# Kernel tuning notes

Measured on AMD Instinct MI355X. Metric: run time of the kernel, lower is better.

The kernel has to match this reference:

```python
import jax, jax.numpy as jnp
import numpy as np
import math

HIDDEN = 1024
N_HEADS = 16
N_KV = 4
HEAD_DIM = HIDDEN // N_HEADS  # 64
B, S = 2, 2048
THETA = 100000.0


def _freqs_cos_sin(dim, end, theta):
    # yarn params: original_max_position_embeddings=2048 >= end, so no ramp scaling,
    # attention_factor=1.0 -> plain RoPE frequencies.
    inv = 1.0 / theta ** (np.arange(0, dim, 2)[: dim // 2] / dim)
    t = np.arange(end)
    f = np.outer(t, inv).astype(np.float32)  # (end, dim/2)
    cos = np.concatenate([np.cos(f), np.cos(f)], axis=-1)  # (end, dim)
    sin = np.concatenate([np.sin(f), np.sin(f)], axis=-1)
    return jnp.asarray(cos), jnp.asarray(sin)


def _rotate(x):
    # stack([-x[...,1::2], x[...,::2]], -1).reshape_as(x)
    return jnp.stack([-x[..., 1::2], x[..., ::2]], axis=-1).reshape(x.shape)


def setup_inputs() -> dict:
    key = jax.random.key(0)
    ks = jax.random.split(key, 9)
    s = 0.02
    return {
        "hidden_states": jax.random.normal(ks[0], (B, S, HIDDEN), jnp.float32),
        "attention_mask": jnp.ones((B, S), jnp.int32),
        "Wq": jax.random.normal(ks[1], (HIDDEN, HIDDEN), jnp.float32) * s,
        "bq": jnp.zeros((HIDDEN,), jnp.float32),
        "Wk": jax.random.normal(ks[2], (HIDDEN, N_KV * HEAD_DIM), jnp.float32) * s,
        "bk": jnp.zeros((N_KV * HEAD_DIM,), jnp.float32),
        "Wv": jax.random.normal(ks[3], (HIDDEN, N_KV * HEAD_DIM), jnp.float32) * s,
        "bv": jnp.zeros((N_KV * HEAD_DIM,), jnp.float32),
        "Wo": jax.random.normal(ks[4], (HIDDEN, HIDDEN), jnp.float32) * s,
        "bo": jnp.zeros((HIDDEN,), jnp.float32),
    }


def reference(hidden_states, attention_mask, Wq, bq, Wk, bk, Wv, bv, Wo, bo):
    b, s, _ = hidden_states.shape
    q = (hidden_states @ Wq + bq).reshape(b, s, N_HEADS, HEAD_DIM)
    k = (hidden_states @ Wk + bk).reshape(b, s, N_KV, HEAD_DIM)
    v = (hidden_states @ Wv + bv).reshape(b, s, N_KV, HEAD_DIM)

    cos, sin = _freqs_cos_sin(HEAD_DIM, s, THETA)
    cos = cos[:, None, :]  # (s,1,d) broadcasts over (b,s,h,d)
    sin = sin[:, None, :]
    q = q * cos + _rotate(q) * sin
    k = k * cos + _rotate(k) * sin

    # GQA: repeat_interleave kv heads -> jnp.repeat along head axis
    rep = N_HEADS // N_KV
    k = jnp.repeat(k, rep, axis=2)
    v = jnp.repeat(v, rep, axis=2)

    scores = jnp.einsum("bqhd,bkhd->bhqk", q, k) / math.sqrt(HEAD_DIM)
    neg = jnp.finfo(scores.dtype).min
    causal = jnp.triu(jnp.ones((s, s), bool), k=1)  # (q,kv)
    bias = jnp.where(causal, neg, 0.0).astype(scores.dtype)[None, None]
    key_mask = attention_mask.astype(bool)[:, None, None, :]  # (b,1,1,kv)
    bias = jnp.where(key_mask, bias, neg)
    probs = jax.nn.softmax(scores + bias, axis=-1)
    attn = jnp.einsum("bhqk,bkhd->bqhd", probs, v).reshape(b, s, HIDDEN)
    return attn @ Wo + bo
```

## Files before the change

kernel.cpp:

```cpp
#include <hip/hip_runtime.h>
#include <cstddef>
#include <cstdint>

#define B_   2
#define S_   2048
#define HID  1024
#define NH_  16
#define NKV_ 4
#define DH_  64
#define ROWS (B_ * S_)
#define NQKV 1536
#define QSCALE 0.18033688011112042f

typedef __bf16 bf16_t;
typedef _Float16 f16_t;
typedef bf16_t bf16x8 __attribute__((ext_vector_type(8)));
typedef bf16_t bf16x4 __attribute__((ext_vector_type(4)));
typedef f16_t  f16x8  __attribute__((ext_vector_type(8)));
typedef f16_t  f16x4  __attribute__((ext_vector_type(4)));
typedef float  f32x4  __attribute__((ext_vector_type(4)));

typedef __attribute__((address_space(1))) const uint32_t gu32_t;
typedef __attribute__((address_space(3))) uint32_t lu32_t;

__device__ __forceinline__ void gl_lds16(const void* g, void* l) {
  __builtin_amdgcn_global_load_lds((gu32_t*)g, (lu32_t*)l, 16, 0, 0);
}

__global__ void prep_all(const float* __restrict__ hs,
                         const float* __restrict__ Wq, const float* __restrict__ Wk,
                         const float* __restrict__ Wv, const float* __restrict__ Wo,
                         const float* __restrict__ bq, const float* __restrict__ bk,
                         const float* __restrict__ bv,
                         bf16_t* __restrict__ hsb,
                         bf16_t* __restrict__ Wt, bf16_t* __restrict__ Wot,
                         float* __restrict__ ball, float2* __restrict__ lut)
{
  const int bid = blockIdx.x;
  if (bid < 2048) {
    const int i = (bid * 256 + threadIdx.x) * 8;
    float4 a = *(const float4*)(hs + i);
    float4 b = *(const float4*)(hs + i + 4);
    bf16x8 o;
    o[0]=(bf16_t)a.x; o[1]=(bf16_t)a.y; o[2]=(bf16_t)a.z; o[3]=(bf16_t)a.w;
    o[4]=(bf16_t)b.x; o[5]=(bf16_t)b.y; o[6]=(bf16_t)b.z; o[7]=(bf16_t)b.w;
    *(bf16x8*)(hsb + i) = o;
    return;
  }
  if (bid >= 4614) {
    const int idx = (bid - 4614) * 256 + threadIdx.x;
    const int s = idx >> 5, j = idx & 31;
    const float L = 0.51905126482615037f;
    const float ang = (float)s * exp2f(-L * (float)j);
    lut[idx] = make_float2(cosf(ang), sinf(ang));
    return;
  }
  if (bid >= 4608) {
    int i = (bid - 4608) * 256 + threadIdx.x;
    if (i < NQKV) ball[i] = (i < 1024) ? bq[i] : ((i < 1280) ? bk[i-1024] : bv[i-1280]);
    return;
  }
  const int wb = bid - 2048;
  const float* src; bf16_t* dst; int N, n0, k0;
  if (wb < 1024)      { src = Wq; dst = Wt;            N = 1024; int t = wb;      n0=(t&31)*32; k0=(t>>5)*32; }
  else if (wb < 1280) { src = Wk; dst = Wt + 1024*HID; N = 256;  int t = wb-1024; n0=(t&7)*32;  k0=(t>>3)*32; }
  else if (wb < 1536) { src = Wv; dst = Wt + 1280*HID; N = 256;  int t = wb-1280; n0=(t&7)*32;  k0=(t>>3)*32; }
  else                { src = Wo; dst = Wot;           N = 1024; int t = wb-1536; n0=(t&31)*32; k0=(t>>5)*32; }
  __shared__ bf16_t T[32][33];
  const int tx = threadIdx.x & 31, ty = threadIdx.x >> 5;
#pragma unroll
  for (int i = 0; i < 4; ++i)
    T[ty + i*8][tx] = (bf16_t)src[(size_t)(k0 + ty + i*8) * N + n0 + tx];
  __syncthreads();
#pragma unroll
  for (int i = 0; i < 4; ++i)
    dst[(size_t)(n0 + ty + i*8) * HID + k0 + tx] = T[tx][ty + i*8];
}

__global__ __launch_bounds__(256, 3) void gemm64_b16o(
    const bf16_t* __restrict__ A, const bf16_t* __restrict__ Bt,
    const float* __restrict__ bias, bf16_t* __restrict__ C, int N)
{
  __shared__ bf16_t As[128 * 64];
  __shared__ bf16_t Bs[64 * 64];
  const int tid  = threadIdx.x;
  const int w    = tid >> 6;
  const int lane = tid & 63;
  const int m    = lane & 15;
  const int quad = lane >> 4;
  const int wm   = w >> 1, wn = w & 1;
  const size_t bm = (size_t)blockIdx.y * 128;
  const size_t bn = (size_t)blockIdx.x * 64;

  const int srow = w * 8 + (lane >> 3);
  const int scol = (lane & 7) * 8;
  const bf16_t* Ag = A  + (bm + srow) * HID + scol;
  const bf16_t* Bg = Bt + (bn + srow) * HID + scol;

  f32x4 acc[4][2];
#pragma unroll
  for (int i = 0; i < 4; ++i)
#pragma unroll
    for (int j = 0; j < 2; ++j) acc[i][j] = (f32x4){0.f, 0.f, 0.f, 0.f};

  for (int k0 = 0; k0 < HID; k0 += 64) {
    __syncthreads();
#pragma unroll
    for (int i = 0; i < 4; ++i)
      gl_lds16(Ag + (size_t)(i * 32) * HID + k0, &As[(w * 8 + i * 32) * 64]);
#pragma unroll
    for (int i = 0; i < 2; ++i)
      gl_lds16(Bg + (size_t)(i * 32) * HID + k0, &Bs[(w * 8 + i * 32) * 64]);
    __syncthreads();
#pragma unroll
    for (int ks = 0; ks < 2; ++ks) {
      bf16x8 af[4], bfr[2];
#pragma unroll
      for (int mt = 0; mt < 4; ++mt)
        af[mt] = *(const bf16x8*)&As[(wm * 64 + mt * 16 + m) * 64 + ks * 32 + quad * 8];
#pragma unroll
      for (int nt = 0; nt < 2; ++nt)
        bfr[nt] = *(const bf16x8*)&Bs[(wn * 32 + nt * 16 + m) * 64 + ks * 32 + quad * 8];
#pragma unroll
      for (int mt = 0; mt < 4; ++mt)
#pragma unroll
        for (int nt = 0; nt < 2; ++nt)
          acc[mt][nt] = __builtin_amdgcn_mfma_f32_16x16x32_bf16(bfr[nt], af[mt], acc[mt][nt], 0, 0, 0);
    }
  }
#pragma unroll
  for (int mt = 0; mt < 4; ++mt) {
    const size_t row = bm + wm * 64 + mt * 16 + m;
#pragma unroll
    for (int nt = 0; nt < 2; ++nt) {
      const size_t col = bn + wn * 32 + nt * 16 + quad * 4;
      float4 bb = *(const float4*)&bias[col];
      bf16x4 o;
      o[0] = (bf16_t)(acc[mt][nt][0] + bb.x);
      o[1] = (bf16_t)(acc[mt][nt][1] + bb.y);
      o[2] = (bf16_t)(acc[mt][nt][2] + bb.z);
      o[3] = (bf16_t)(acc[mt][nt][3] + bb.w);
      *(bf16x4*)&C[row * N + col] = o;
    }
  }
}

__global__ __launch_bounds__(256, 3) void gemm64_f32o(
    const bf16_t* __restrict__ A, const bf16_t* __restrict__ Bt,
    const float* __restrict__ bias, float* __restrict__ C, int N)
{
  __shared__ bf16_t As[128 * 64];
  __shared__ bf16_t Bs[64 * 64];
  const int tid  = threadIdx.x;
  const int w    = tid >> 6;
  const int lane = tid & 63;
  const int m    = lane & 15;
  const int quad = lane >> 4;
  const int wm   = w >> 1, wn = w & 1;
  const size_t bm = (size_t)blockIdx.y * 128;
  const size_t bn = (size_t)blockIdx.x * 64;

  const int srow = w * 8 + (lane >> 3);
  const int scol = (lane & 7) * 8;
  const bf16_t* Ag = A  + (bm + srow) * HID + scol;
  const bf16_t* Bg = Bt + (bn + srow) * HID + scol;

  f32x4 acc[4][2];
#pragma unroll
  for (int i = 0; i < 4; ++i)
#pragma unroll
    for (int j = 0; j < 2; ++j) acc[i][j] = (f32x4){0.f, 0.f, 0.f, 0.f};

  for (int k0 = 0; k0 < HID; k0 += 64) {
    __syncthreads();
#pragma unroll
    for (int i = 0; i < 4; ++i)
      gl_lds16(Ag + (size_t)(i * 32) * HID + k0, &As[(w * 8 + i * 32) * 64]);
#pragma unroll
    for (int i = 0; i < 2; ++i)
      gl_lds16(Bg + (size_t)(i * 32) * HID + k0, &Bs[(w * 8 + i * 32) * 64]);
    __syncthreads();
#pragma unroll
    for (int ks = 0; ks < 2; ++ks) {
      bf16x8 af[4], bfr[2];
#pragma unroll
      for (int mt = 0; mt < 4; ++mt)
        af[mt] = *(const bf16x8*)&As[(wm * 64 + mt * 16 + m) * 64 + ks * 32 + quad * 8];
#pragma unroll
      for (int nt = 0; nt < 2; ++nt)
        bfr[nt] = *(const bf16x8*)&Bs[(wn * 32 + nt * 16 + m) * 64 + ks * 32 + quad * 8];
#pragma unroll
      for (int mt = 0; mt < 4; ++mt)
#pragma unroll
        for (int nt = 0; nt < 2; ++nt)
          acc[mt][nt] = __builtin_amdgcn_mfma_f32_16x16x32_bf16(bfr[nt], af[mt], acc[mt][nt], 0, 0, 0);
    }
  }
#pragma unroll
  for (int mt = 0; mt < 4; ++mt) {
    const size_t row = bm + wm * 64 + mt * 16 + m;
#pragma unroll
    for (int nt = 0; nt < 2; ++nt) {
      const size_t col = bn + wn * 32 + nt * 16 + quad * 4;
      float4 bb = *(const float4*)&bias[col];
      float4 o;
      o.x = acc[mt][nt][0] + bb.x; o.y = acc[mt][nt][1] + bb.y;
      o.z = acc[mt][nt][2] + bb.z; o.w = acc[mt][nt][3] + bb.w;
      *(float4*)&C[row * N + col] = o;
    }
  }
}

__global__ void prep_kv(const bf16_t* __restrict__ QKVb, const float2* __restrict__ lut,
                        bf16_t* __restrict__ Kimg, f16_t* __restrict__ Vimg)
{
  __shared__ bf16_t Lk[64][72];
  __shared__ bf16_t Lv[64][72];
  const int bid = blockIdx.x, t = threadIdx.x;
  const int kt = bid & 31, kvh = (bid >> 5) & 3, b = bid >> 7;
  const size_t img = ((size_t)(b * NKV_ + kvh) * 32 + kt) * 4096;

  {
    const int r0 = t >> 3, c8 = (t & 7) * 8;
#pragma unroll
    for (int i = 0; i < 2; ++i) {
      const int r = r0 + i * 32;
      const bf16_t* src = QKVb + (size_t)(b * S_ + kt * 64 + r) * NQKV + 1024 + kvh * DH_ + c8;
      *(bf16x8*)&Lk[r][c8] = *(const bf16x8*)src;
      *(bf16x8*)&Lv[r][c8] = *(const bf16x8*)(src + 256);
    }
  }
  __syncthreads();
  {
    const int key = t & 63, cg = t >> 6;
    const int srow = kt * 64 + key;
    bf16x8 a = *(const bf16x8*)&Lk[key][cg * 16];
    bf16x8 c = *(const bf16x8*)&Lk[key][cg * 16 + 8];
    const float2* lp = lut + srow * 32 + ((cg & 1) * 16);
    float v[16];
#pragma unroll
    for (int i = 0; i < 8; ++i) { v[i] = (float)a[i]; v[i + 8] = (float)c[i]; }
    bf16x8 o0, o1;
#pragma unroll
    for (int j = 0; j < 8; ++j) {
      const float2 ce = lp[2 * j], co = lp[2 * j + 1];
      const float y0 = v[2*j] * ce.x - v[2*j+1] * ce.y;
      const float y1 = v[2*j+1] * co.x + v[2*j] * co.y;
      if (j < 4) { o0[2*j] = (bf16_t)y0; o0[2*j+1] = (bf16_t)y1; }
      else       { o1[2*(j-4)] = (bf16_t)y0; o1[2*(j-4)+1] = (bf16_t)y1; }
    }
    const int s0 = (2 * cg) ^ (key & 7);
    *(bf16x8*)&Kimg[img + key * 64 + s0 * 8]       = o0;
    *(bf16x8*)&Kimg[img + key * 64 + (s0 ^ 1) * 8] = o1;
  }
  {
    const int d = t & 63, cg = t >> 6;
#pragma unroll
    for (int g4 = 0; g4 < 4; ++g4) {
      const int g = cg * 4 + g4;
      f16x4 o;
#pragma unroll
      for (int j = 0; j < 4; ++j)
        o[j] = (f16_t)(float)Lv[g * 4 + j][d];
      const int slot = g ^ (d & 15);
      *(f16x4*)&Vimg[img + d * 64 + slot * 4] = o;
    }
  }
}

__global__ __launch_bounds__(64) void attn_v5(
    const bf16_t* __restrict__ QKVb, const float2* __restrict__ lut,
    const bf16_t* __restrict__ Kt2, const f16_t* __restrict__ Vt2,
    const int* __restrict__ amask, bf16_t* __restrict__ Ab)
{
  __shared__ __align__(16) bf16_t Ks[64 * 64];
  __shared__ __align__(16) f16_t  Vs[64 * 64];

  const int lane = threadIdx.x;
  const int m    = lane & 15;
  const int quad = lane >> 4;
  const int h    = blockIdx.y;
  const int b    = blockIdx.z;
  const int kvh  = h >> 2;
  const int qt   = 63 - blockIdx.x;
  const int q0w  = qt * 32;
  const int nkt  = ((q0w + 31) >> 6) + 1;

  bf16x8 aq[2][2];
#pragma unroll
  for (int mt = 0; mt < 2; ++mt) {
    const int spos = q0w + mt * 16 + m;
    const bf16_t* qsrc = QKVb + (size_t)(b * S_ + spos) * NQKV + h * DH_;
    float2 l8[8];
#pragma unroll
    for (int j = 0; j < 8; ++j) l8[j] = lut[spos * 32 + quad * 8 + j];
#pragma unroll
    for (int kc = 0; kc < 2; ++kc) {
      bf16x8 x = *(const bf16x8*)(qsrc + kc * 32 + quad * 8);
      bf16x8 y;
#pragma unroll
      for (int i = 0; i < 4; ++i) {
        const float x0 = (float)x[2*i], x1 = (float)x[2*i+1];
        y[2*i]   = (bf16_t)((x0 * l8[2*i].x   - x1 * l8[2*i].y)   * QSCALE);
        y[2*i+1] = (bf16_t)((x1 * l8[2*i+1].x + x0 * l8[2*i+1].y) * QSCALE);
      }
      aq[mt][kc] = y;
    }
  }

  f32x4 oacc[2][4];
#pragma unroll
  for (int mt = 0; mt < 2; ++mt)
#pragma unroll
    for (int d = 0; d < 4; ++d) oacc[mt][d] = (f32x4){0.f,0.f,0.f,0.f};
  float lpart[2] = {0.f, 0.f};

  const size_t imgbase = ((size_t)(b * NKV_ + kvh) * 32) * 4096;
  const bf16_t* Kg = Kt2 + imgbase;
  const f16_t*  Vg = Vt2 + imgbase;
  const int x0s = quad ^ (m & 7);
  const int x1s = (4 + quad) ^ (m & 7);
  const int* amp = amask + b * S_;

  for (int kt = 0; kt < nkt; ++kt) {
    const int kbase = kt * 64;
#pragma unroll
    for (int i = 0; i < 8; ++i)
      gl_lds16(Kg + (size_t)kt * 4096 + i * 512 + lane * 8, &Ks[i * 512]);
#pragma unroll
    for (int i = 0; i < 8; ++i)
      gl_lds16(Vg + (size_t)kt * 4096 + i * 512 + lane * 8, &Vs[i * 512]);

    const uint64_t mb = __ballot(amp[kbase + lane] != 0);
    __builtin_amdgcn_s_waitcnt(0x0F70);

    f32x4 sc[2][4];
#pragma unroll
    for (int mt = 0; mt < 2; ++mt)
#pragma unroll
      for (int cb = 0; cb < 4; ++cb) sc[mt][cb] = (f32x4){0.f,0.f,0.f,0.f};
#pragma unroll
    for (int cb = 0; cb < 4; ++cb) {
      const bf16x8 bk0 = *(const bf16x8*)&Ks[(cb*16 + m) * 64 + x0s * 8];
      const bf16x8 bk1 = *(const bf16x8*)&Ks[(cb*16 + m) * 64 + x1s * 8];
#pragma unroll
      for (int mt = 0; mt < 2; ++mt) {
        sc[mt][cb] = __builtin_amdgcn_mfma_f32_16x16x32_bf16(bk0, aq[mt][0], sc[mt][cb], 0, 0, 0);
        sc[mt][cb] = __builtin_amdgcn_mfma_f32_16x16x32_bf16(bk1, aq[mt][1], sc[mt][cb], 0, 0, 0);
      }
    }

    f16x4 bp[2][4];
#pragma unroll
    for (int mt = 0; mt < 2; ++mt) {
      const bool needm = (kbase + 63 > q0w + mt*16) || (mb != ~0ull);
      if (needm) {
        const int qv = q0w + mt*16 + m;
#pragma unroll
        for (int cb = 0; cb < 4; ++cb)
#pragma unroll
          for (int r = 0; r < 4; ++r) {
            const int idx = cb*16 + quad*4 + r;
            const bool ok = (kbase + idx <= qv) && ((mb >> idx) & 1);
            sc[mt][cb][r] = ok ? sc[mt][cb][r] : -1e38f;
          }
      }
      float sum = 0.f;
#pragma unroll
      for (int cb = 0; cb < 4; ++cb) {
        f16x4 pp;
#pragma unroll
        for (int r = 0; r < 4; ++r) {
          const float p = exp2f(sc[mt][cb][r]);
          sum += p;
          pp[r] = (f16_t)p;
        }
        bp[mt][cb] = pp;
      }
      lpart[mt] += sum;
    }

#pragma unroll
    for (int cb = 0; cb < 4; ++cb) {
      f16x4 av[4];
#pragma unroll
      for (int dblk = 0; dblk < 4; ++dblk) {
        const int slot = (cb * 4 + quad) ^ m;
        av[dblk] = *(const f16x4*)&Vs[(dblk*16 + m) * 64 + slot * 4];
      }
#pragma unroll
      for (int mt = 0; mt < 2; ++mt)
#pragma unroll
        for (int dblk = 0; dblk < 4; ++dblk)
          oacc[mt][dblk] = __builtin_amdgcn_mfma_f32_16x16x16f16(av[dblk], bp[mt][cb], oacc[mt][dblk], 0, 0, 0);
    }
  }

#pragma unroll
  for (int mt = 0; mt < 2; ++mt) {
    float l = lpart[mt];
    l += __shfl_xor(l, 16);
    l += __shfl_xor(l, 32);
    const float inv = 1.0f / l;
    const size_t row = (size_t)(b * S_ + q0w + mt*16 + m);
#pragma unroll
    for (int dblk = 0; dblk < 4; ++dblk) {
      bf16x4 o;
      o[0] = (bf16_t)(oacc[mt][dblk][0] * inv);
      o[1] = (bf16_t)(oacc[mt][dblk][1] * inv);
      o[2] = (bf16_t)(oacc[mt][dblk][2] * inv);
      o[3] = (bf16_t)(oacc[mt][dblk][3] * inv);
      *(bf16x4*)&Ab[row * HID + h * DH_ + dblk * 16 + quad * 4] = o;
    }
  }
}

extern "C" void kernel_launch(void* const* d_in, const int* in_sizes, int n_in,
                              void* d_out, int out_size, void* d_ws, size_t ws_size,
                              hipStream_t stream)
{
  const float* hs    = (const float*)d_in[0];
  const int*   amask = (const int*)  d_in[1];
  const float* Wq    = (const float*)d_in[2];
  const float* bq    = (const float*)d_in[3];
  const float* Wk    = (const float*)d_in[4];
  const float* bk    = (const float*)d_in[5];
  const float* Wv    = (const float*)d_in[6];
  const float* bv    = (const float*)d_in[7];
  const float* Wo    = (const float*)d_in[8];
  const float* bo    = (const float*)d_in[9];
  float* out = (float*)d_out;

  bf16_t* QKVb = (bf16_t*)d_ws;
  bf16_t* hsb  = QKVb + (size_t)ROWS * NQKV;
  bf16_t* Wt   = hsb + (size_t)ROWS * HID;
  bf16_t* Wot  = Wt + (size_t)NQKV * HID;
  float*  ball = (float*)(Wot + (size_t)HID * HID);
  bf16_t* Kimg = (bf16_t*)(ball + NQKV);
  f16_t*  Vimg = (f16_t*)(Kimg + (size_t)B_*NKV_*32*4096);
  float2* lut  = (float2*)(Vimg + (size_t)B_*NKV_*32*4096);
  bf16_t* Ab   = hsb;

  prep_all<<<4870, 256, 0, stream>>>(hs, Wq, Wk, Wv, Wo, bq, bk, bv,
                                     hsb, Wt, Wot, ball, lut);

  gemm64_b16o<<<dim3(NQKV/64, ROWS/128), 256, 0, stream>>>(hsb, Wt, ball, QKVb, NQKV);

  prep_kv<<<256, 256, 0, stream>>>(QKVb, lut, Kimg, Vimg);

  attn_v5<<<dim3(64, NH_, B_), 64, 0, stream>>>(QKVb, lut, Kimg, Vimg, amask, Ab);

  gemm64_f32o<<<dim3(HID/64, ROWS/128), 256, 0, stream>>>(Ab, Wot, bo, out, HID);
}
```

Before: 212.7 us.

## Load K/V MFMA fragments directly into registers with double-buffered prefetch

The attention kernel no longer stages K/V tiles through LDS. Each lane now loads its MFMA fragments straight from global memory into registers, using two register buffers so the next tile's loads overlap the current tile's compute. prep_kv rewrites the K and V images into a fragment-friendly unswizzled layout so each lane's reads are contiguous, and it reads K directly from global memory instead of through shared memory. This removes the LDS round trip and waitcnt stalls, at the cost of more VGPRs for two fragment sets, which could lower occupancy.

```diff
diff --git a/kernel.cpp b/kernel.cpp
--- a/kernel.cpp
+++ b/kernel.cpp
@@ -214,7 +214,6 @@
 __global__ void prep_kv(const bf16_t* __restrict__ QKVb, const float2* __restrict__ lut,
                         bf16_t* __restrict__ Kimg, f16_t* __restrict__ Vimg)
 {
-  __shared__ bf16_t Lk[64][72];
   __shared__ bf16_t Lv[64][72];
   const int bid = blockIdx.x, t = threadIdx.x;
   const int kt = bid & 31, kvh = (bid >> 5) & 3, b = bid >> 7;
@@ -225,17 +224,16 @@
 #pragma unroll
     for (int i = 0; i < 2; ++i) {
       const int r = r0 + i * 32;
-      const bf16_t* src = QKVb + (size_t)(b * S_ + kt * 64 + r) * NQKV + 1024 + kvh * DH_ + c8;
-      *(bf16x8*)&Lk[r][c8] = *(const bf16x8*)src;
-      *(bf16x8*)&Lv[r][c8] = *(const bf16x8*)(src + 256);
-    }
-  }
-  __syncthreads();
+      const bf16_t* src = QKVb + (size_t)(b * S_ + kt * 64 + r) * NQKV + 1280 + kvh * DH_ + c8;
+      *(bf16x8*)&Lv[r][c8] = *(const bf16x8*)src;
+    }
+  }
   {
     const int key = t & 63, cg = t >> 6;
     const int srow = kt * 64 + key;
-    bf16x8 a = *(const bf16x8*)&Lk[key][cg * 16];
-    bf16x8 c = *(const bf16x8*)&Lk[key][cg * 16 + 8];
+    const bf16_t* p = QKVb + (size_t)(b * S_ + srow) * NQKV + 1024 + kvh * DH_ + cg * 16;
+    bf16x8 a = *(const bf16x8*)p;
+    bf16x8 c = *(const bf16x8*)(p + 8);
     const float2* lp = lut + srow * 32 + ((cg & 1) * 16);
     float v[16];
 #pragma unroll
@@ -249,10 +247,10 @@
       if (j < 4) { o0[2*j] = (bf16_t)y0; o0[2*j+1] = (bf16_t)y1; }
       else       { o1[2*(j-4)] = (bf16_t)y0; o1[2*(j-4)+1] = (bf16_t)y1; }
     }
-    const int s0 = (2 * cg) ^ (key & 7);
-    *(bf16x8*)&Kimg[img + key * 64 + s0 * 8]       = o0;
-    *(bf16x8*)&Kimg[img + key * 64 + (s0 ^ 1) * 8] = o1;
-  }
+    *(bf16x8*)&Kimg[img + key * 64 + cg * 16]     = o0;
+    *(bf16x8*)&Kimg[img + key * 64 + cg * 16 + 8] = o1;
+  }
+  __syncthreads();
   {
     const int d = t & 63, cg = t >> 6;
 #pragma unroll
@@ -262,20 +260,97 @@
 #pragma unroll
       for (int j = 0; j < 4; ++j)
         o[j] = (f16_t)(float)Lv[g * 4 + j][d];
-      const int slot = g ^ (d & 15);
-      *(f16x4*)&Vimg[img + d * 64 + slot * 4] = o;
-    }
-  }
-}
-
-__global__ __launch_bounds__(64) void attn_v5(
+      *(f16x4*)&Vimg[img + (d * 4 + (g & 3)) * 16 + (g >> 2) * 4] = o;
+    }
+  }
+}
+
+struct KVFrag {
+  bf16x8 k[4][2];
+  f16x4  v[4][4];
+};
+
+__device__ __forceinline__ void load_frags(const bf16_t* __restrict__ Kg,
+                                           const f16_t* __restrict__ Vg,
+                                           int kt, int m, int quad, KVFrag& f)
+{
+  const bf16_t* kp = Kg + (size_t)kt * 4096 + m * 64 + quad * 8;
+#pragma unroll
+  for (int cb = 0; cb < 4; ++cb)
+#pragma unroll
+    for (int kc = 0; kc < 2; ++kc)
+      f.k[cb][kc] = *(const bf16x8*)(kp + cb * 1024 + kc * 32);
+  const f16_t* vp = Vg + (size_t)kt * 4096 + (m * 4 + quad) * 16;
+#pragma unroll
+  for (int dblk = 0; dblk < 4; ++dblk)
+#pragma unroll
+    for (int c2 = 0; c2 < 2; ++c2) {
+      f16x8 t = *(const f16x8*)(vp + dblk * 1024 + c2 * 8);
+      f.v[dblk][c2*2]   = __builtin_shufflevector(t, t, 0, 1, 2, 3);
+      f.v[dblk][c2*2+1] = __builtin_shufflevector(t, t, 4, 5, 6, 7);
+    }
+}
+
+__device__ __forceinline__ void tile_compute(const KVFrag& f, int mreg, int kbase,
+    int q0w, int m, int quad, const bf16x8 (&aq)[2][2],
+    f32x4 (&oacc)[2][4], float (&lpart)[2])
+{
+  const uint64_t mb = __ballot(mreg != 0);
+  f32x4 sc[2][4];
+#pragma unroll
+  for (int mt = 0; mt < 2; ++mt)
+#pragma unroll
+    for (int cb = 0; cb < 4; ++cb) sc[mt][cb] = (f32x4){0.f,0.f,0.f,0.f};
+#pragma unroll
+  for (int cb = 0; cb < 4; ++cb)
+#pragma unroll
+    for (int mt = 0; mt < 2; ++mt) {
+      sc[mt][cb] = __builtin_amdgcn_mfma_f32_16x16x32_bf16(f.k[cb][0], aq[mt][0], sc[mt][cb], 0, 0, 0);
+      sc[mt][cb] = __builtin_amdgcn_mfma_f32_16x16x32_bf16(f.k[cb][1], aq[mt][1], sc[mt][cb], 0, 0, 0);
+    }
+  f16x4 bp[2][4];
+#pragma unroll
+  for (int mt = 0; mt < 2; ++mt) {
+    const bool needm = (kbase + 63 > q0w + mt*16) || (mb != ~0ull);
+    if (needm) {
+      const int qv = q0w + mt*16 + m;
+#pragma unroll
+      for (int cb = 0; cb < 4; ++cb)
+#pragma unroll
+        for (int r = 0; r < 4; ++r) {
+          const int idx = cb*16 + quad*4 + r;
+          const bool ok = (kbase + idx <= qv) && ((mb >> idx) & 1);
+          sc[mt][cb][r] = ok ? sc[mt][cb][r] : -1e38f;
+        }
+    }
+    float sum = 0.f;
+#pragma unroll
+    for (int cb = 0; cb < 4; ++cb) {
+      f16x4 pp;
+#pragma unroll
+      for (int r = 0; r < 4; ++r) {
+        const float p = exp2f(sc[mt][cb][r]);
+        sum += p;
+        pp[r] = (f16_t)p;
+      }
+      bp[mt][cb] = pp;
+    }
+    lpart[mt] += sum;
+  }
+#pragma unroll
+  for (int cb = 0; cb < 4; ++cb)
+#pragma unroll
+    for (int mt = 0; mt < 2; ++mt)
+#pragma unroll
+      for (int dblk = 0; dblk < 4; ++dblk)
+        oacc[mt][dblk] = __builtin_amdgcn_mfma_f32_16x16x16f16(f.v[dblk][cb], bp[mt][cb], oacc[mt][dblk], 0, 0, 0);
+}
+
+__global__ __launch_bounds__(64) void attn_v7(
     const bf16_t* __restrict__ QKVb, const float2* __restrict__ lut,
     const bf16_t* __restrict__ Kt2, const f16_t* __restrict__ Vt2,
     const int* __restrict__ amask, bf16_t* __restrict__ Ab)
 {
-  __shared__ __align__(16) bf16_t Ks[64 * 64];
-  __shared__ __align__(16) f16_t  Vs[64 * 64];
-
   const int lane = threadIdx.x;
   const int m    = lane & 15;
   const int quad = lane >> 4;
@@ -318,82 +393,19 @@
   const size_t imgbase = ((size_t)(b * NKV_ + kvh) * 32) * 4096;
   const bf16_t* Kg = Kt2 + imgbase;
   const f16_t*  Vg = Vt2 + imgbase;
-  const int x0s = quad ^ (m & 7);
-  const int x1s = (4 + quad) ^ (m & 7);
   const int* amp = amask + b * S_;
 
-  for (int kt = 0; kt < nkt; ++kt) {
-    const int kbase = kt * 64;
-#pragma unroll
-    for (int i = 0; i < 8; ++i)
-      gl_lds16(Kg + (size_t)kt * 4096 + i * 512 + lane * 8, &Ks[i * 512]);
-#pragma unroll
-    for (int i = 0; i < 8; ++i)
-      gl_lds16(Vg + (size_t)kt * 4096 + i * 512 + lane * 8, &Vs[i * 512]);
-
-    const uint64_t mb = __ballot(amp[kbase + lane] != 0);
-    __builtin_amdgcn_s_waitcnt(0x0F70);
-
-    f32x4 sc[2][4];
-#pragma unroll
-    for (int mt = 0; mt < 2; ++mt)
-#pragma unroll
-      for (int cb = 0; cb < 4; ++cb) sc[mt][cb] = (f32x4){0.f,0.f,0.f,0.f};
-#pragma unroll
-    for (int cb = 0; cb < 4; ++cb) {
-      const bf16x8 bk0 = *(const bf16x8*)&Ks[(cb*16 + m) * 64 + x0s * 8];
-      const bf16x8 bk1 = *(const bf16x8*)&Ks[(cb*16 + m) * 64 + x1s * 8];
-#pragma unroll
-      for (int mt = 0; mt < 2; ++mt) {
-        sc[mt][cb] = __builtin_amdgcn_mfma_f32_16x16x32_bf16(bk0, aq[mt][0], sc[mt][cb], 0, 0, 0);
-        sc[mt][cb] = __builtin_amdgcn_mfma_f32_16x16x32_bf16(bk1, aq[mt][1], sc[mt][cb], 0, 0, 0);
-      }
-    }
-
-    f16x4 bp[2][4];
-#pragma unroll
-    for (int mt = 0; mt < 2; ++mt) {
-      const bool needm = (kbase + 63 > q0w + mt*16) || (mb != ~0ull);
-      if (needm) {
-        const int qv = q0w + mt*16 + m;
-#pragma unroll
-        for (int cb = 0; cb < 4; ++cb)
-#pragma unroll
-          for (int r = 0; r < 4; ++r) {
-            const int idx = cb*16 + quad*4 + r;
-            const bool ok = (kbase + idx <= qv) && ((mb >> idx) & 1);
-            sc[mt][cb][r] = ok ? sc[mt][cb][r] : -1e38f;
-          }
-      }
-      float sum = 0.f;
-#pragma unroll
-      for (int cb = 0; cb < 4; ++cb) {
-        f16x4 pp;
-#pragma unroll
-        for (int r = 0; r < 4; ++r) {
-          const float p = exp2f(sc[mt][cb][r]);
-          sum += p;
-          pp[r] = (f16_t)p;
-        }
-        bp[mt][cb] = pp;
-      }
-      lpart[mt] += sum;
-    }
-
-#pragma unroll
-    for (int cb = 0; cb < 4; ++cb) {
-      f16x4 av[4];
-#pragma unroll
-      for (int dblk = 0; dblk < 4; ++dblk) {
-        const int slot = (cb * 4 + quad) ^ m;
-        av[dblk] = *(const f16x4*)&Vs[(dblk*16 + m) * 64 + slot * 4];
-      }
-#pragma unroll
-      for (int mt = 0; mt < 2; ++mt)
-#pragma unroll
-        for (int dblk = 0; dblk < 4; ++dblk)
-          oacc[mt][dblk] = __builtin_amdgcn_mfma_f32_16x16x16f16(av[dblk], bp[mt][cb], oacc[mt][dblk], 0, 0, 0);
-    }
+  KVFrag fA, fB;
+  load_frags(Kg, Vg, 0, m, quad, fA);
+  int m0 = amp[lane];
+  int m1 = 0;
+  for (int kt = 0; kt < nkt; kt += 2) {
+    const bool h1 = (kt + 1 < nkt);
+    if (h1) { load_frags(Kg, Vg, kt + 1, m, quad, fB); m1 = amp[(kt + 1) * 64 + lane]; }
+    tile_compute(fA, m0, kt * 64, q0w, m, quad, aq, oacc, lpart);
+    if (!h1) break;
+    if (kt + 2 < nkt) { load_frags(Kg, Vg, kt + 2, m, quad, fA); m0 = amp[(kt + 2) * 64 + lane]; }
+    tile_compute(fB, m1, (kt + 1) * 64, q0w, m, quad, aq, oacc, lpart);
   }
 
 #pragma unroll
@@ -448,7 +460,7 @@
 
   prep_kv<<<256, 256, 0, stream>>>(QKVb, lut, Kimg, Vimg);
 
-  attn_v5<<<dim3(64, NH_, B_), 64, 0, stream>>>(QKVb, lut, Kimg, Vimg, amask, Ab);
+  attn_v7<<<dim3(64, NH_, B_), 64, 0, stream>>>(QKVb, lut, Kimg, Vimg, amask, Ab);
 
   gemm64_f32o<<<dim3(HID/64, ROWS/128), 256, 0, stream>>>(Ab, Wot, bo, out, HID);
 }
```

Result: slower. 255.6 us (+20.1%).

## Double-buffer GEMM tiles and share K/V across GQA heads in attention

Applied to the files above, without the earlier changes.

Both projection GEMMs now keep two shared-memory tile buffers: the first k-tile is loaded before the loop, and each iteration issues the next tile's loads before computing on the current one, which removes one barrier per step. The attention kernel changes from one 64-thread block per query head to one 256-thread block per KV head. Its four waves each handle one query head of the group, loading K/V tiles cooperatively into double-buffered shared memory and prefetching the next attention-mask value. The aim is to overlap global-to-LDS traffic with MFMA work and cut redundant K/V loads by four. In exchange the kernels use twice the LDS and a larger attention block, which may reduce occupancy.

```diff
diff --git a/kernel.cpp b/kernel.cpp
--- a/kernel.cpp
+++ b/kernel.cpp
@@ -81,8 +81,8 @@
     const bf16_t* __restrict__ A, const bf16_t* __restrict__ Bt,
     const float* __restrict__ bias, bf16_t* __restrict__ C, int N)
 {
-  __shared__ bf16_t As[128 * 64];
-  __shared__ bf16_t Bs[64 * 64];
+  __shared__ bf16_t As[2][128 * 64];
+  __shared__ bf16_t Bs[2][64 * 64];
   const int tid  = threadIdx.x;
   const int w    = tid >> 6;
   const int lane = tid & 63;
@@ -103,30 +103,40 @@
 #pragma unroll
     for (int j = 0; j < 2; ++j) acc[i][j] = (f32x4){0.f, 0.f, 0.f, 0.f};
 
+#pragma unroll
+  for (int i = 0; i < 4; ++i)
+    gl_lds16(Ag + (size_t)(i * 32) * HID, &As[0][(w * 8 + i * 32) * 64]);
+#pragma unroll
+  for (int i = 0; i < 2; ++i)
+    gl_lds16(Bg + (size_t)(i * 32) * HID, &Bs[0][(w * 8 + i * 32) * 64]);
+
+  int p = 0;
   for (int k0 = 0; k0 < HID; k0 += 64) {
     __syncthreads();
-#pragma unroll
-    for (int i = 0; i < 4; ++i)
-      gl_lds16(Ag + (size_t)(i * 32) * HID + k0, &As[(w * 8 + i * 32) * 64]);
-#pragma unroll
-    for (int i = 0; i < 2; ++i)
-      gl_lds16(Bg + (size_t)(i * 32) * HID + k0, &Bs[(w * 8 + i * 32) * 64]);
-    __syncthreads();
+    if (k0 + 64 < HID) {
+#pragma unroll
+      for (int i = 0; i < 4; ++i)
+        gl_lds16(Ag + (size_t)(i * 32) * HID + k0 + 64, &As[p^1][(w * 8 + i * 32) * 64]);
+#pragma unroll
+      for (int i = 0; i < 2; ++i)
+        gl_lds16(Bg + (size_t)(i * 32) * HID + k0 + 64, &Bs[p^1][(w * 8 + i * 32) * 64]);
+    }
 #pragma unroll
     for (int ks = 0; ks < 2; ++ks) {
       bf16x8 af[4], bfr[2];
 #pragma unroll
       for (int mt = 0; mt < 4; ++mt)
-        af[mt] = *(const bf16x8*)&As[(wm * 64 + mt * 16 + m) * 64 + ks * 32 + quad * 8];
+        af[mt] = *(const bf16x8*)&As[p][(wm * 64 + mt * 16 + m) * 64 + ks * 32 + quad * 8];
 #pragma unroll
       for (int nt = 0; nt < 2; ++nt)
-        bfr[nt] = *(const bf16x8*)&Bs[(wn * 32 + nt * 16 + m) * 64 + ks * 32 + quad * 8];
+        bfr[nt] = *(const bf16x8*)&Bs[p][(wn * 32 + nt * 16 + m) * 64 + ks * 32 + quad * 8];
 #pragma unroll
       for (int mt = 0; mt < 4; ++mt)
 #pragma unroll
         for (int nt = 0; nt < 2; ++nt)
           acc[mt][nt] = __builtin_amdgcn_mfma_f32_16x16x32_bf16(bfr[nt], af[mt], acc[mt][nt], 0, 0, 0);
     }
+    p ^= 1;
   }
 #pragma unroll
   for (int mt = 0; mt < 4; ++mt) {
@@ -149,8 +159,8 @@
     const bf16_t* __restrict__ A, const bf16_t* __restrict__ Bt,
     const float* __restrict__ bias, float* __restrict__ C, int N)
 {
-  __shared__ bf16_t As[128 * 64];
-  __shared__ bf16_t Bs[64 * 64];
+  __shared__ bf16_t As[2][128 * 64];
+  __shared__ bf16_t Bs[2][64 * 64];
   const int tid  = threadIdx.x;
   const int w    = tid >> 6;
   const int lane = tid & 63;
@@ -171,30 +181,40 @@
 #pragma unroll
     for (int j = 0; j < 2; ++j) acc[i][j] = (f32x4){0.f, 0.f, 0.f, 0.f};
 
+#pragma unroll
+  for (int i = 0; i < 4; ++i)
+    gl_lds16(Ag + (size_t)(i * 32) * HID, &As[0][(w * 8 + i * 32) * 64]);
+#pragma unroll
+  for (int i = 0; i < 2; ++i)
+    gl_lds16(Bg + (size_t)(i * 32) * HID, &Bs[0][(w * 8 + i * 32) * 64]);
+
+  int p = 0;
   for (int k0 = 0; k0 < HID; k0 += 64) {
     __syncthreads();
-#pragma unroll
-    for (int i = 0; i < 4; ++i)
-      gl_lds16(Ag + (size_t)(i * 32) * HID + k0, &As[(w * 8 + i * 32) * 64]);
-#pragma unroll
-    for (int i = 0; i < 2; ++i)
-      gl_lds16(Bg + (size_t)(i * 32) * HID + k0, &Bs[(w * 8 + i * 32) * 64]);
-    __syncthreads();
+    if (k0 + 64 < HID) {
+#pragma unroll
+      for (int i = 0; i < 4; ++i)
+        gl_lds16(Ag + (size_t)(i * 32) * HID + k0 + 64, &As[p^1][(w * 8 + i * 32) * 64]);
+#pragma unroll
+      for (int i = 0; i < 2; ++i)
+        gl_lds16(Bg + (size_t)(i * 32) * HID + k0 + 64, &Bs[p^1][(w * 8 + i * 32) * 64]);
+    }
 #pragma unroll
     for (int ks = 0; ks < 2; ++ks) {
       bf16x8 af[4], bfr[2];
 #pragma unroll
       for (int mt = 0; mt < 4; ++mt)
-        af[mt] = *(const bf16x8*)&As[(wm * 64 + mt * 16 + m) * 64 + ks * 32 + quad * 8];
+        af[mt] = *(const bf16x8*)&As[p][(wm * 64 + mt * 16 + m) * 64 + ks * 32 + quad * 8];
 #pragma unroll
       for (int nt = 0; nt < 2; ++nt)
-        bfr[nt] = *(const bf16x8*)&Bs[(wn * 32 + nt * 16 + m) * 64 + ks * 32 + quad * 8];
+        bfr[nt] = *(const bf16x8*)&Bs[p][(wn * 32 + nt * 16 + m) * 64 + ks * 32 + quad * 8];
 #pragma unroll
       for (int mt = 0; mt < 4; ++mt)
 #pragma unroll
         for (int nt = 0; nt < 2; ++nt)
           acc[mt][nt] = __builtin_amdgcn_mfma_f32_16x16x32_bf16(bfr[nt], af[mt], acc[mt][nt], 0, 0, 0);
     }
+    p ^= 1;
   }
 #pragma unroll
   for (int mt = 0; mt < 4; ++mt) {
@@ -268,20 +288,22 @@
   }
 }
 
-__global__ __launch_bounds__(64) void attn_v5(
+__global__ __launch_bounds__(256, 2) void attn_v6(
     const bf16_t* __restrict__ QKVb, const float2* __restrict__ lut,
     const bf16_t* __restrict__ Kt2, const f16_t* __restrict__ Vt2,
     const int* __restrict__ amask, bf16_t* __restrict__ Ab)
 {
-  __shared__ __align__(16) bf16_t Ks[64 * 64];
-  __shared__ __align__(16) f16_t  Vs[64 * 64];
-
-  const int lane = threadIdx.x;
+  __shared__ __align__(16) bf16_t Ks[2][64 * 64];
+  __shared__ __align__(16) f16_t  Vs[2][64 * 64];
+
+  const int tid  = threadIdx.x;
+  const int w    = tid >> 6;
+  const int lane = tid & 63;
   const int m    = lane & 15;
   const int quad = lane >> 4;
-  const int h    = blockIdx.y;
+  const int kvh  = blockIdx.y;
   const int b    = blockIdx.z;
-  const int kvh  = h >> 2;
+  const int h    = kvh * 4 + w;
   const int qt   = 63 - blockIdx.x;
   const int q0w  = qt * 32;
   const int nkt  = ((q0w + 31) >> 6) + 1;
@@ -322,17 +344,26 @@
   const int x1s = (4 + quad) ^ (m & 7);
   const int* amp = amask + b * S_;
 
+  gl_lds16(Kg + (2*w)   * 512 + lane * 8, &Ks[0][(2*w)   * 512]);
+  gl_lds16(Kg + (2*w+1) * 512 + lane * 8, &Ks[0][(2*w+1) * 512]);
+  gl_lds16(Vg + (2*w)   * 512 + lane * 8, &Vs[0][(2*w)   * 512]);
+  gl_lds16(Vg + (2*w+1) * 512 + lane * 8, &Vs[0][(2*w+1) * 512]);
+  int mcur = amp[lane];
+
+  int p = 0;
   for (int kt = 0; kt < nkt; ++kt) {
     const int kbase = kt * 64;
-#pragma unroll
-    for (int i = 0; i < 8; ++i)
-      gl_lds16(Kg + (size_t)kt * 4096 + i * 512 + lane * 8, &Ks[i * 512]);
-#pragma unroll
-    for (int i = 0; i < 8; ++i)
-      gl_lds16(Vg + (size_t)kt * 4096 + i * 512 + lane * 8, &Vs[i * 512]);
-
-    const uint64_t mb = __ballot(amp[kbase + lane] != 0);
-    __builtin_amdgcn_s_waitcnt(0x0F70);
+    __syncthreads();
+    const bool more = (kt + 1 < nkt);
+    if (more) {
+      const size_t off = (size_t)(kt + 1) * 4096;
+      gl_lds16(Kg + off + (2*w)   * 512 + lane * 8, &Ks[p^1][(2*w)   * 512]);
+      gl_lds16(Kg + off + (2*w+1) * 512 + lane * 8, &Ks[p^1][(2*w+1) * 512]);
+      gl_lds16(Vg + off + (2*w)   * 512 + lane * 8, &Vs[p^1][(2*w)   * 512]);
+      gl_lds16(Vg + off + (2*w+1) * 512 + lane * 8, &Vs[p^1][(2*w+1) * 512]);
+    }
+    int mnext = more ? amp[(kt + 1) * 64 + lane] : 0;
+    const uint64_t mb = __ballot(mcur != 0);
 
     f32x4 sc[2][4];
 #pragma unroll
@@ -341,8 +372,8 @@
       for (int cb = 0; cb < 4; ++cb) sc[mt][cb] = (f32x4){0.f,0.f,0.f,0.f};
 #pragma unroll
     for (int cb = 0; cb < 4; ++cb) {
-      const bf16x8 bk0 = *(const bf16x8*)&Ks[(cb*16 + m) * 64 + x0s * 8];
-      const bf16x8 bk1 = *(const bf16x8*)&Ks[(cb*16 + m) * 64 + x1s * 8];
+      const bf16x8 bk0 = *(const bf16x8*)&Ks[p][(cb*16 + m) * 64 + x0s * 8];
+      const bf16x8 bk1 = *(const bf16x8*)&Ks[p][(cb*16 + m) * 64 + x1s * 8];
 #pragma unroll
       for (int mt = 0; mt < 2; ++mt) {
         sc[mt][cb] = __builtin_amdgcn_mfma_f32_16x16x32_bf16(bk0, aq[mt][0], sc[mt][cb], 0, 0, 0);
@@ -371,9 +402,9 @@
         f16x4 pp;
 #pragma unroll
         for (int r = 0; r < 4; ++r) {
-          const float p = exp2f(sc[mt][cb][r]);
-          sum += p;
-          pp[r] = (f16_t)p;
+          const float pv = exp2f(sc[mt][cb][r]);
+          sum += pv;
+          pp[r] = (f16_t)pv;
         }
         bp[mt][cb] = pp;
       }
@@ -386,7 +417,7 @@
 #pragma unroll
       for (int dblk = 0; dblk < 4; ++dblk) {
         const int slot = (cb * 4 + quad) ^ m;
-        av[dblk] = *(const f16x4*)&Vs[(dblk*16 + m) * 64 + slot * 4];
+        av[dblk] = *(const f16x4*)&Vs[p][(dblk*16 + m) * 64 + slot * 4];
       }
 #pragma unroll
       for (int mt = 0; mt < 2; ++mt)
@@ -394,6 +425,8 @@
         for (int dblk = 0; dblk < 4; ++dblk)
           oacc[mt][dblk] = __builtin_amdgcn_mfma_f32_16x16x16f16(av[dblk], bp[mt][cb], oacc[mt][dblk], 0, 0, 0);
     }
+    mcur = mnext;
+    p ^= 1;
   }
 
 #pragma unroll
@@ -448,7 +481,7 @@
 
   prep_kv<<<256, 256, 0, stream>>>(QKVb, lut, Kimg, Vimg);
 
-  attn_v5<<<dim3(64, NH_, B_), 64, 0, stream>>>(QKVb, lut, Kimg, Vimg, amask, Ab);
+  attn_v6<<<dim3(64, NKV_, B_), 256, 0, stream>>>(QKVb, lut, Kimg, Vimg, amask, Ab);
 
   gemm64_f32o<<<dim3(HID/64, ROWS/128), 256, 0, stream>>>(Ab, Wot, bo, out, HID);
 }
```

New measurement: 208.0 us. 2.2% less time.
